# Kernel optimization log

Hardware: AMD Instinct MI355X
Metric: run time of the kernel (lower is better)

Reference implementation:

```python
import jax, jax.numpy as jnp
import numpy as np
import math

DT_SCALE = 1.0
DT_MIN, DT_MAX = 0.001, 0.1


def setup_inputs() -> dict:
    key = jax.random.key(0)
    ku, kdt, ka, kb, kc = jax.random.split(key, 5)
    batch, seq_len, d_model, d_state = 32, 4096, 256, 64
    u = jax.random.normal(ku, (batch, seq_len, d_model), dtype=jnp.float32)
    # log_dt ~ U[log(dt_min), log(dt_max)]
    log_dt = jax.random.uniform(kdt, (d_model,), dtype=jnp.float32) * (
        math.log(DT_MAX) - math.log(DT_MIN)) + math.log(DT_MIN)
    # A_real = -exp(U(-1, 1))  (strictly negative -> stable recurrence)
    A_real = -jnp.exp(jax.random.uniform(ka, (d_model, d_state), dtype=jnp.float32) * 2.0 - 1.0)
    B = jax.random.normal(kb, (d_model, d_state), dtype=jnp.float32)
    C = jax.random.normal(kc, (d_model, d_state), dtype=jnp.float32)
    x0 = jnp.zeros((d_model, d_state), dtype=jnp.float32)
    return {"u": u, "log_dt": log_dt, "A_real": A_real, "B": B, "C": C, "x0": x0}


def reference(u, log_dt, A_real, B, C, x0):
    # u: (batch, seq_len, d_model)
    batch = u.shape[0]
    dt = jnp.exp(log_dt) * DT_SCALE                      # (D,)
    A_tilde = jnp.exp(A_real * dt[:, None])              # (D, N)
    B_tilde = (1.0 - A_tilde) * B / A_real               # (D, N)
    x_init = jnp.broadcast_to(x0, (batch,) + x0.shape)   # (B, D, N)

    def step(x, u_t):
        # x: (B, D, N), u_t: (B, D)
        x = A_tilde * x + B_tilde * u_t[..., None]
        y = jnp.sum(C * x, axis=-1)                      # (B, D)
        return x, y

    u_t_major = jnp.swapaxes(u, 0, 1)                    # (L, B, D)
    _, ys = jax.lax.scan(step, x_init, u_t_major)        # ys: (L, B, D)
    return jnp.swapaxes(ys, 0, 1)                        # (B, L, D)
```

## Files before the change

### kernel.cpp

```cpp
#include <hip/hip_runtime.h>
#include <math.h>

#define BATCH 32
#define SEQ   4096
#define DM    256
#define NS    64
#define TSTEP 16


__global__ __launch_bounds__(256, 2)
void pass1_kernel(const float* __restrict__ u,
                  const float* __restrict__ log_dt,
                  const float* __restrict__ A_real,
                  float* __restrict__ S, int Tc) {
    __shared__ float tiles[4][2][TSTEP][16];
    int wid  = threadIdx.x >> 6;
    int lane = threadIdx.x & 63;
    int wave = (blockIdx.x * blockDim.x + threadIdx.x) >> 6;
    int w  = wave & 511;
    int g  = wave >> 9;
    int b  = w >> 4;
    int d0 = (w & 15) << 4;
    int c   = lane >> 2;
    int sub = lane & 3;
    int d   = d0 + c;
    int n0  = sub << 4;

    float a[16], z[16];
    {
        float dt = expf(log_dt[d]);
        const float* Ap = A_real + d * NS + n0;
#pragma unroll
        for (int k = 0; k < 16; ++k) {
            a[k] = expf(Ap[k] * dt);
            z[k] = 0.0f;
        }
    }

    const float* gsrc = u + (size_t)b * SEQ * DM + (size_t)(g * Tc) * DM
                        + (size_t)(lane >> 2) * DM + d0 + ((lane & 3) << 2);
    const size_t tadv = (size_t)TSTEP * DM;
    float* slot0 = &tiles[wid][0][0][0] + (lane << 2);
    const int ntiles = Tc / TSTEP;

    float4 rnext = *(const float4*)gsrc;
    *(float4*)slot0 = rnext;
    gsrc += tadv;
    rnext = *(const float4*)gsrc;
    gsrc += tadv;

    for (int tile = 0; tile < ntiles; ++tile) {
        int cur = tile & 1;
        if (tile + 1 < ntiles)
            *(float4*)(slot0 + (((tile + 1) & 1) << 8)) = rnext;
        if (tile + 2 < ntiles) {
            rnext = *(const float4*)gsrc;
            gsrc += tadv;
        }
        const float* tb = &tiles[wid][cur][0][0] + c;
#pragma unroll
        for (int s = 0; s < TSTEP; ++s) {
            float uv = tb[s << 4];
#pragma unroll
            for (int k = 0; k < 16; ++k)
                z[k] = fmaf(a[k], z[k], uv);
        }
    }

    float* Sp = S + (((size_t)g * BATCH + b) * DM + d) * NS + n0;
    float4* Sp4 = (float4*)Sp;
#pragma unroll
    for (int j = 0; j < 4; ++j)
        Sp4[j] = make_float4(z[4 * j], z[4 * j + 1], z[4 * j + 2], z[4 * j + 3]);
}

__global__ void pass2_kernel(float* __restrict__ S,
                             const float* __restrict__ log_dt,
                             const float* __restrict__ A_real,
                             const float* __restrict__ B,
                             const float* __restrict__ x0,
                             int C, int Tc) {
    int idx = blockIdx.x * blockDim.x + threadIdx.x;
    if (idx >= BATCH * DM * NS) return;
    int dn = idx & (DM * NS - 1);
    int d = dn >> 6;
    float ar = A_real[dn];
    float dt = expf(log_dt[d]);
    float aT = expf(ar * dt * (float)Tc);
    float x0v = x0[dn];
    float prev;
    if (x0v == 0.0f) {
        prev = 0.0f;
    } else {
        float at = expf(ar * dt);
        float bt = (1.0f - at) * B[dn] / ar;
        prev = (bt != 0.0f) ? (x0v / bt) : 0.0f;
    }
    const size_t stride = (size_t)BATCH * DM * NS;
    if (C == 16) {
        float v[15];
#pragma unroll
        for (int g = 0; g < 15; ++g) v[g] = S[(size_t)g * stride + idx];
#pragma unroll
        for (int g = 0; g < 15; ++g) {
            S[(size_t)g * stride + idx] = prev;
            prev = fmaf(aT, prev, v[g]);
        }
        S[15 * stride + idx] = prev;
    } else {
        for (int g = 0; g < C - 1; ++g) {
            float* p = S + (size_t)g * stride + idx;
            float s = *p;
            *p = prev;
            prev = fmaf(aT, prev, s);
        }
        S[(size_t)(C - 1) * stride + idx] = prev;
    }
}

__global__ __launch_bounds__(256, 2)
void pass3_kernel(const float* __restrict__ u,
                  const float* __restrict__ log_dt,
                  const float* __restrict__ A_real,
                  const float* __restrict__ B,
                  const float* __restrict__ Cm,
                  const float* __restrict__ S,
                  const float* __restrict__ x0,
                  float* __restrict__ y, int Tc, int useS) {
    __shared__ float tiles[4][2][TSTEP][16];
    int wid  = threadIdx.x >> 6;
    int lane = threadIdx.x & 63;
    int wave = (blockIdx.x * blockDim.x + threadIdx.x) >> 6;
    int w  = wave & 511;
    int g  = wave >> 9;
    int b  = w >> 4;
    int d0 = (w & 15) << 4;
    int c   = lane >> 2;
    int sub = lane & 3;
    int d   = d0 + c;
    int n0  = sub << 4;

    float a[16], cbt[16], z[16];
    {
        float dt = expf(log_dt[d]);
        const float* Ap = A_real + d * NS + n0;
        const float* Bp = B + d * NS + n0;
        const float* Cp = Cm + d * NS + n0;
#pragma unroll
        for (int k = 0; k < 16; ++k) {
            float ar = Ap[k];
            float at = expf(ar * dt);
            a[k] = at;
            cbt[k] = Cp[k] * ((1.0f - at) * Bp[k] / ar);
        }
        if (useS) {
            const float4* Sp4 = (const float4*)(S +
                (((size_t)g * BATCH + b) * DM + d) * NS + n0);
#pragma unroll
            for (int j = 0; j < 4; ++j) {
                float4 v = Sp4[j];
                z[4 * j] = v.x; z[4 * j + 1] = v.y;
                z[4 * j + 2] = v.z; z[4 * j + 3] = v.w;
            }
        } else {
            const float* Xp = x0 + d * NS + n0;
#pragma unroll
            for (int k = 0; k < 16; ++k) {
                float x0v = Xp[k];
                if (x0v == 0.0f) { z[k] = 0.0f; }
                else {
                    float bt = (1.0f - a[k]) * Bp[k] / Ap[k];
                    z[k] = (bt != 0.0f) ? (x0v / bt) : 0.0f;
                }
            }
        }
    }

    const float* gsrc = u + (size_t)b * SEQ * DM + (size_t)(g * Tc) * DM
                        + (size_t)(lane >> 2) * DM + d0 + ((lane & 3) << 2);
    const size_t tadv = (size_t)TSTEP * DM;
    float* slot0 = &tiles[wid][0][0][0] + (lane << 2);
    const int ntiles = Tc / TSTEP;
    float* yptr = y + (size_t)b * SEQ * DM + (size_t)(g * Tc) * DM + d;

    float4 rnext = *(const float4*)gsrc;
    *(float4*)slot0 = rnext;
    gsrc += tadv;
    rnext = *(const float4*)gsrc;
    gsrc += tadv;

    for (int tile = 0; tile < ntiles; ++tile) {
        int cur = tile & 1;
        if (tile + 1 < ntiles)
            *(float4*)(slot0 + (((tile + 1) & 1) << 8)) = rnext;
        if (tile + 2 < ntiles) {
            rnext = *(const float4*)gsrc;
            gsrc += tadv;
        }
        const float* tb = &tiles[wid][cur][0][0] + c;
#pragma unroll
        for (int s = 0; s < TSTEP; ++s) {
            float uv = tb[s << 4];
            float p0 = 0.0f, p1 = 0.0f;
#pragma unroll
            for (int k = 0; k < 16; k += 2) {
                z[k]     = fmaf(a[k],     z[k],     uv); p0 = fmaf(cbt[k],     z[k],     p0);
                z[k + 1] = fmaf(a[k + 1], z[k + 1], uv); p1 = fmaf(cbt[k + 1], z[k + 1], p1);
            }
            float p = p0 + p1;
            p += __shfl_xor(p, 1);
            p += __shfl_xor(p, 2);
            if (sub == 0) *yptr = p;
            yptr += DM;
        }
    }
}

extern "C" void kernel_launch(void* const* d_in, const int* in_sizes, int n_in,
                              void* d_out, int out_size, void* d_ws, size_t ws_size,
                              hipStream_t stream) {
    const float* u      = (const float*)d_in[0];
    const float* log_dt = (const float*)d_in[1];
    const float* A_real = (const float*)d_in[2];
    const float* B      = (const float*)d_in[3];
    const float* Cm     = (const float*)d_in[4];
    const float* x0     = (const float*)d_in[5];
    float* y = (float*)d_out;
    float* S = (float*)d_ws;

    const size_t per_chunk = (size_t)BATCH * DM * NS * sizeof(float);
    int C = 16;
    while (C > 1 && (size_t)C * per_chunk > ws_size) C >>= 1;
    if ((size_t)C * per_chunk > ws_size) C = 1;
    int Tc = SEQ / C;

    if (C > 1) {
        pass1_kernel<<<dim3((C - 1) * 128), dim3(256), 0, stream>>>(
            u, log_dt, A_real, S, Tc);
        pass2_kernel<<<dim3((BATCH * DM * NS) / 256), dim3(256), 0, stream>>>(
            S, log_dt, A_real, B, x0, C, Tc);
    }
    pass3_kernel<<<dim3(C * 128), dim3(256), 0, stream>>>(
        u, log_dt, A_real, B, Cm, S, x0, y, Tc, (C > 1) ? 1 : 0);
}
```

Before: 388.4 us.

## Fuse scan passes into one cooperative kernel with grid-wide sync

Adds a cooperative kernel that runs the chunk-summary pass, a grid sync, then a per-wave carry combine and the output pass. It drops the separate carry-propagation kernel and two extra launches. The price is redundant carry accumulation over earlier chunks in every wave and a grid barrier. It falls back to the three-kernel path when the occupancy check says all blocks cannot be co-resident.

Measured after the change: 397.7 us. 2.4% more time.

```diff
diff --git a/kernel.cpp b/kernel.cpp
--- a/kernel.cpp
+++ b/kernel.cpp
@@ -1,5 +1,8 @@
 #include <hip/hip_runtime.h>
+#include <hip/hip_cooperative_groups.h>
 #include <math.h>
+
+namespace cg = cooperative_groups;
 
 #define BATCH 32
 #define SEQ   4096
@@ -7,6 +10,155 @@
 #define NS    64
 #define TSTEP 16
 
+
+__global__ __launch_bounds__(256, 2)
+void fused_kernel(const float* __restrict__ u,
+                  const float* __restrict__ log_dt,
+                  const float* __restrict__ A_real,
+                  const float* __restrict__ B,
+                  const float* __restrict__ Cm,
+                  float* __restrict__ S,
+                  const float* __restrict__ x0,
+                  float* __restrict__ y, int Tc, int C) {
+    __shared__ float tiles[4][2][TSTEP][16];
+    int wid  = threadIdx.x >> 6;
+    int lane = threadIdx.x & 63;
+    int wave = (blockIdx.x * blockDim.x + threadIdx.x) >> 6;
+    int w  = wave & 511;
+    int g  = wave >> 9;
+    int b  = w >> 4;
+    int d0 = (w & 15) << 4;
+    int c   = lane >> 2;
+    int sub = lane & 3;
+    int d   = d0 + c;
+    int n0  = sub << 4;
+
+    float dt = expf(log_dt[d]);
+    const float* Ap = A_real + d * NS + n0;
+    float a[16], z[16];
+#pragma unroll
+    for (int k = 0; k < 16; ++k)
+        a[k] = expf(Ap[k] * dt);
+
+    const size_t tadv = (size_t)TSTEP * DM;
+    float* slot0 = &tiles[wid][0][0][0] + (lane << 2);
+    const int ntiles = Tc / TSTEP;
+    const size_t estride = (size_t)BATCH * DM * NS;
+
+    if (C > 1 && g < C - 1) {
+#pragma unroll
+        for (int k = 0; k < 16; ++k) z[k] = 0.0f;
+        const float* gsrc = u + (size_t)b * SEQ * DM + (size_t)(g * Tc) * DM
+                            + (size_t)(lane >> 2) * DM + d0 + ((lane & 3) << 2);
+        float4 rnext = *(const float4*)gsrc;
+        *(float4*)slot0 = rnext;
+        gsrc += tadv;
+        rnext = *(const float4*)gsrc;
+        gsrc += tadv;
+        for (int tile = 0; tile < ntiles; ++tile) {
+            int cur = tile & 1;
+            if (tile + 1 < ntiles)
+                *(float4*)(slot0 + (((tile + 1) & 1) << 8)) = rnext;
+            if (tile + 2 < ntiles) {
+                rnext = *(const float4*)gsrc;
+                gsrc += tadv;
+            }
+            const float* tb = &tiles[wid][cur][0][0] + c;
+#pragma unroll
+            for (int s = 0; s < TSTEP; ++s) {
+                float uv = tb[s << 4];
+#pragma unroll
+                for (int k = 0; k < 16; ++k)
+                    z[k] = fmaf(a[k], z[k], uv);
+            }
+        }
+        float* Sp = S + (((size_t)g * BATCH + b) * DM + d) * NS + n0;
+        float4* Sp4 = (float4*)Sp;
+#pragma unroll
+        for (int j = 0; j < 4; ++j)
+            Sp4[j] = make_float4(z[4*j], z[4*j+1], z[4*j+2], z[4*j+3]);
+    }
+
+    cg::this_grid().sync();
+
+    {
+        const float* Xp = x0 + d * NS + n0;
+        const float* Bp = B + d * NS + n0;
+#pragma unroll
+        for (int k = 0; k < 16; ++k) {
+            float x0v = Xp[k];
+            if (x0v == 0.0f) { z[k] = 0.0f; }
+            else {
+                float bt = (1.0f - a[k]) * Bp[k] / Ap[k];
+                z[k] = (bt != 0.0f) ? (x0v / bt) : 0.0f;
+            }
+        }
+    }
+    if (g > 0) {
+        float aT[16];
+        float dTc = dt * (float)Tc;
+#pragma unroll
+        for (int k = 0; k < 16; ++k)
+            aT[k] = expf(Ap[k] * dTc);
+        const float* Eb = S + ((size_t)b * DM + d) * NS + n0;
+        for (int h = 0; h < g; ++h) {
+            const float4* E4 = (const float4*)(Eb + (size_t)h * estride);
+            float e[16];
+#pragma unroll
+            for (int j = 0; j < 4; ++j) {
+                float4 v = E4[j];
+                e[4*j] = v.x; e[4*j+1] = v.y; e[4*j+2] = v.z; e[4*j+3] = v.w;
+            }
+#pragma unroll
+            for (int k = 0; k < 16; ++k)
+                z[k] = fmaf(aT[k], z[k], e[k]);
+        }
+    }
+
+    float cbt[16];
+    {
+        const float* Bp = B + d * NS + n0;
+        const float* Cp = Cm + d * NS + n0;
+#pragma unroll
+        for (int k = 0; k < 16; ++k)
+            cbt[k] = Cp[k] * ((1.0f - a[k]) * Bp[k] / Ap[k]);
+    }
+    const float* gsrc = u + (size_t)b * SEQ * DM + (size_t)(g * Tc) * DM
+                        + (size_t)(lane >> 2) * DM + d0 + ((lane & 3) << 2);
+    float* yptr = y + (size_t)b * SEQ * DM + (size_t)(g * Tc) * DM + d;
+
+    float4 rnext = *(const float4*)gsrc;
+    *(float4*)slot0 = rnext;
+    gsrc += tadv;
+    rnext = *(const float4*)gsrc;
+    gsrc += tadv;
+
+    for (int tile = 0; tile < ntiles; ++tile) {
+        int cur = tile & 1;
+        if (tile + 1 < ntiles)
+            *(float4*)(slot0 + (((tile + 1) & 1) << 8)) = rnext;
+        if (tile + 2 < ntiles) {
+            rnext = *(const float4*)gsrc;
+            gsrc += tadv;
+        }
+        const float* tb = &tiles[wid][cur][0][0] + c;
+#pragma unroll
+        for (int s = 0; s < TSTEP; ++s) {
+            float uv = tb[s << 4];
+            float p0 = 0.0f, p1 = 0.0f;
+#pragma unroll
+            for (int k = 0; k < 16; k += 2) {
+                z[k]   = fmaf(a[k],   z[k],   uv); p0 = fmaf(cbt[k],   z[k],   p0);
+                z[k+1] = fmaf(a[k+1], z[k+1], uv); p1 = fmaf(cbt[k+1], z[k+1], p1);
+            }
+            float p = p0 + p1;
+            p += __shfl_xor(p, 1);
+            p += __shfl_xor(p, 2);
+            if (sub == 0) yptr[s * DM] = p;
+        }
+        yptr += tadv;
+    }
+}
 
 __global__ __launch_bounds__(256, 2)
 void pass1_kernel(const float* __restrict__ u,
@@ -36,7 +188,6 @@
             z[k] = 0.0f;
         }
     }
-
     const float* gsrc = u + (size_t)b * SEQ * DM + (size_t)(g * Tc) * DM
                         + (size_t)(lane >> 2) * DM + d0 + ((lane & 3) << 2);
     const size_t tadv = (size_t)TSTEP * DM;
@@ -66,12 +217,11 @@
                 z[k] = fmaf(a[k], z[k], uv);
         }
     }
-
     float* Sp = S + (((size_t)g * BATCH + b) * DM + d) * NS + n0;
     float4* Sp4 = (float4*)Sp;
 #pragma unroll
     for (int j = 0; j < 4; ++j)
-        Sp4[j] = make_float4(z[4 * j], z[4 * j + 1], z[4 * j + 2], z[4 * j + 3]);
+        Sp4[j] = make_float4(z[4*j], z[4*j+1], z[4*j+2], z[4*j+3]);
 }
 
 __global__ void pass2_kernel(float* __restrict__ S,
@@ -159,8 +309,7 @@
 #pragma unroll
             for (int j = 0; j < 4; ++j) {
                 float4 v = Sp4[j];
-                z[4 * j] = v.x; z[4 * j + 1] = v.y;
-                z[4 * j + 2] = v.z; z[4 * j + 3] = v.w;
+                z[4*j] = v.x; z[4*j+1] = v.y; z[4*j+2] = v.z; z[4*j+3] = v.w;
             }
         } else {
             const float* Xp = x0 + d * NS + n0;
@@ -204,8 +353,8 @@
             float p0 = 0.0f, p1 = 0.0f;
 #pragma unroll
             for (int k = 0; k < 16; k += 2) {
-                z[k]     = fmaf(a[k],     z[k],     uv); p0 = fmaf(cbt[k],     z[k],     p0);
-                z[k + 1] = fmaf(a[k + 1], z[k + 1], uv); p1 = fmaf(cbt[k + 1], z[k + 1], p1);
+                z[k]   = fmaf(a[k],   z[k],   uv); p0 = fmaf(cbt[k],   z[k],   p0);
+                z[k+1] = fmaf(a[k+1], z[k+1], uv); p1 = fmaf(cbt[k+1], z[k+1], p1);
             }
             float p = p0 + p1;
             p += __shfl_xor(p, 1);
@@ -234,6 +383,35 @@
     if ((size_t)C * per_chunk > ws_size) C = 1;
     int Tc = SEQ / C;
 
+    static int coop_state = -1;
+    if (coop_state == -1) {
+        int ok = 0;
+        int dev = 0, nb = 0;
+        hipDeviceProp_t prop;
+        if (hipGetDevice(&dev) == hipSuccess &&
+            hipGetDeviceProperties(&prop, dev) == hipSuccess &&
+            hipOccupancyMaxActiveBlocksPerMultiprocessor(
+                &nb, (const void*)fused_kernel, 256, 0) == hipSuccess) {
+            if (prop.cooperativeLaunch &&
+                (long)nb * prop.multiProcessorCount >= (long)C * 128)
+                ok = 1;
+        }
+        (void)hipGetLastError();
+        coop_state = ok;
+    }
+
+    if (coop_state == 1) {
+        int aTc = Tc, aC = C;
+        void* args[] = {(void*)&u, (void*)&log_dt, (void*)&A_real, (void*)&B,
+                        (void*)&Cm, (void*)&S, (void*)&x0, (void*)&y,
+                        (void*)&aTc, (void*)&aC};
+        hipError_t err = hipLaunchCooperativeKernel(
+            (const void*)fused_kernel, dim3(C * 128), dim3(256), args, 0, stream);
+        if (err == hipSuccess) return;
+        (void)hipGetLastError();
+        coop_state = 0;
+    }
+
     if (C > 1) {
         pass1_kernel<<<dim3((C - 1) * 128), dim3(256), 0, stream>>>(
             u, log_dt, A_real, S, Tc);
```

## Fuse three-pass chunked scan into one kernel with inter-block flag synchronization

Applied to the files above, without the earlier changes.

Replaces the separate pass1/pass2/pass3 launches with a single kernel. Blocks take a dynamic virtual block id from an atomic counter, compute their chunk-end state, publish it with a flag, then wait on the flags of earlier chunks. Each block combines the earlier chunk states itself and runs the output scan. This removes two kernel launches and the separate sequential pass2, but adds spin-waiting, a memset, and a per-block combine of up to 15 chunk states read from global memory.

New measurement: 1.272 ms. 3.28x slower.

```diff
diff --git a/kernel.cpp b/kernel.cpp
--- a/kernel.cpp
+++ b/kernel.cpp
@@ -9,14 +9,26 @@
 
 
 __global__ __launch_bounds__(256, 2)
-void pass1_kernel(const float* __restrict__ u,
+void fused_kernel(const float* __restrict__ u,
                   const float* __restrict__ log_dt,
                   const float* __restrict__ A_real,
-                  float* __restrict__ S, int Tc) {
+                  const float* __restrict__ B,
+                  const float* __restrict__ Cm,
+                  float* __restrict__ S,
+                  const float* __restrict__ x0,
+                  float* __restrict__ y,
+                  unsigned int* __restrict__ flags,
+                  int Tc, int C) {
     __shared__ float tiles[4][2][TSTEP][16];
+    __shared__ int vbid_s;
+    if (threadIdx.x == 0)
+        vbid_s = (int)atomicAdd(&flags[31], 1u);
+    __syncthreads();
+    int vbid = vbid_s;
+
     int wid  = threadIdx.x >> 6;
     int lane = threadIdx.x & 63;
-    int wave = (blockIdx.x * blockDim.x + threadIdx.x) >> 6;
+    int wave = (vbid << 2) | wid;
     int w  = wave & 511;
     int g  = wave >> 9;
     int b  = w >> 4;
@@ -26,22 +38,102 @@
     int d   = d0 + c;
     int n0  = sub << 4;
 
+    float dt = expf(log_dt[d]);
+    const float* Ap = A_real + d * NS + n0;
     float a[16], z[16];
-    {
-        float dt = expf(log_dt[d]);
-        const float* Ap = A_real + d * NS + n0;
-#pragma unroll
-        for (int k = 0; k < 16; ++k) {
-            a[k] = expf(Ap[k] * dt);
-            z[k] = 0.0f;
-        }
-    }
-
-    const float* gsrc = u + (size_t)b * SEQ * DM + (size_t)(g * Tc) * DM
-                        + (size_t)(lane >> 2) * DM + d0 + ((lane & 3) << 2);
+#pragma unroll
+    for (int k = 0; k < 16; ++k)
+        a[k] = expf(Ap[k] * dt);
+
     const size_t tadv = (size_t)TSTEP * DM;
     float* slot0 = &tiles[wid][0][0][0] + (lane << 2);
     const int ntiles = Tc / TSTEP;
+    const size_t estride = (size_t)BATCH * DM * NS;
+
+    if (g < C - 1) {
+#pragma unroll
+        for (int k = 0; k < 16; ++k) z[k] = 0.0f;
+        const float* gsrc = u + (size_t)b * SEQ * DM + (size_t)(g * Tc) * DM
+                            + (size_t)(lane >> 2) * DM + d0 + ((lane & 3) << 2);
+        float4 rnext = *(const float4*)gsrc;
+        *(float4*)slot0 = rnext;
+        gsrc += tadv;
+        rnext = *(const float4*)gsrc;
+        gsrc += tadv;
+        for (int tile = 0; tile < ntiles; ++tile) {
+            int cur = tile & 1;
+            if (tile + 1 < ntiles)
+                *(float4*)(slot0 + (((tile + 1) & 1) << 8)) = rnext;
+            if (tile + 2 < ntiles) {
+                rnext = *(const float4*)gsrc;
+                gsrc += tadv;
+            }
+            const float* tb = &tiles[wid][cur][0][0] + c;
+#pragma unroll
+            for (int s = 0; s < TSTEP; ++s) {
+                float uv = tb[s << 4];
+#pragma unroll
+                for (int k = 0; k < 16; ++k)
+                    z[k] = fmaf(a[k], z[k], uv);
+            }
+        }
+        float* Sp = S + (((size_t)g * BATCH + b) * DM + d) * NS + n0;
+        float4* Sp4 = (float4*)Sp;
+#pragma unroll
+        for (int j = 0; j < 4; ++j)
+            Sp4[j] = make_float4(z[4*j], z[4*j+1], z[4*j+2], z[4*j+3]);
+        __threadfence();
+        if (lane == 0)
+            atomicAdd(&flags[g], 1u);
+    }
+
+    {
+        const float* Xp = x0 + d * NS + n0;
+        const float* Bp = B + d * NS + n0;
+#pragma unroll
+        for (int k = 0; k < 16; ++k) {
+            float x0v = Xp[k];
+            if (x0v == 0.0f) { z[k] = 0.0f; }
+            else {
+                float bt = (1.0f - a[k]) * Bp[k] / Ap[k];
+                z[k] = (bt != 0.0f) ? (x0v / bt) : 0.0f;
+            }
+        }
+    }
+    if (g > 0) {
+        float aT[16];
+        float dTc = dt * (float)Tc;
+#pragma unroll
+        for (int k = 0; k < 16; ++k)
+            aT[k] = expf(Ap[k] * dTc);
+        const float* Eb = S + ((size_t)b * DM + d) * NS + n0;
+        for (int h = 0; h < g; ++h) {
+            while (__hip_atomic_load(&flags[h], __ATOMIC_ACQUIRE,
+                                     __HIP_MEMORY_SCOPE_AGENT) < 512u)
+                __builtin_amdgcn_s_sleep(2);
+            const float4* E4 = (const float4*)(Eb + (size_t)h * estride);
+#pragma unroll
+            for (int j = 0; j < 4; ++j) {
+                float4 v = E4[j];
+                z[4*j]   = fmaf(aT[4*j],   z[4*j],   v.x);
+                z[4*j+1] = fmaf(aT[4*j+1], z[4*j+1], v.y);
+                z[4*j+2] = fmaf(aT[4*j+2], z[4*j+2], v.z);
+                z[4*j+3] = fmaf(aT[4*j+3], z[4*j+3], v.w);
+            }
+        }
+    }
+
+    float cbt[16];
+    {
+        const float* Bp = B + d * NS + n0;
+        const float* Cp = Cm + d * NS + n0;
+#pragma unroll
+        for (int k = 0; k < 16; ++k)
+            cbt[k] = Cp[k] * ((1.0f - a[k]) * Bp[k] / Ap[k]);
+    }
+    const float* gsrc = u + (size_t)b * SEQ * DM + (size_t)(g * Tc) * DM
+                        + (size_t)(lane >> 2) * DM + d0 + ((lane & 3) << 2);
+    float* yptr = y + (size_t)b * SEQ * DM + (size_t)(g * Tc) * DM + d;
 
     float4 rnext = *(const float4*)gsrc;
     *(float4*)slot0 = rnext;
@@ -61,78 +153,34 @@
 #pragma unroll
         for (int s = 0; s < TSTEP; ++s) {
             float uv = tb[s << 4];
-#pragma unroll
-            for (int k = 0; k < 16; ++k)
-                z[k] = fmaf(a[k], z[k], uv);
-        }
-    }
-
-    float* Sp = S + (((size_t)g * BATCH + b) * DM + d) * NS + n0;
-    float4* Sp4 = (float4*)Sp;
-#pragma unroll
-    for (int j = 0; j < 4; ++j)
-        Sp4[j] = make_float4(z[4 * j], z[4 * j + 1], z[4 * j + 2], z[4 * j + 3]);
+            float p0 = 0.0f, p1 = 0.0f;
+#pragma unroll
+            for (int k = 0; k < 16; k += 2) {
+                z[k]   = fmaf(a[k],   z[k],   uv); p0 = fmaf(cbt[k],   z[k],   p0);
+                z[k+1] = fmaf(a[k+1], z[k+1], uv); p1 = fmaf(cbt[k+1], z[k+1], p1);
+            }
+            float p = p0 + p1;
+            p += __shfl_xor(p, 1);
+            p += __shfl_xor(p, 2);
+            if (sub == 0) yptr[s * DM] = p;
+        }
+        yptr += tadv;
+    }
 }
 
-__global__ void pass2_kernel(float* __restrict__ S,
-                             const float* __restrict__ log_dt,
-                             const float* __restrict__ A_real,
-                             const float* __restrict__ B,
-                             const float* __restrict__ x0,
-                             int C, int Tc) {
-    int idx = blockIdx.x * blockDim.x + threadIdx.x;
-    if (idx >= BATCH * DM * NS) return;
-    int dn = idx & (DM * NS - 1);
-    int d = dn >> 6;
-    float ar = A_real[dn];
-    float dt = expf(log_dt[d]);
-    float aT = expf(ar * dt * (float)Tc);
-    float x0v = x0[dn];
-    float prev;
-    if (x0v == 0.0f) {
-        prev = 0.0f;
-    } else {
-        float at = expf(ar * dt);
-        float bt = (1.0f - at) * B[dn] / ar;
-        prev = (bt != 0.0f) ? (x0v / bt) : 0.0f;
-    }
-    const size_t stride = (size_t)BATCH * DM * NS;
-    if (C == 16) {
-        float v[15];
-#pragma unroll
-        for (int g = 0; g < 15; ++g) v[g] = S[(size_t)g * stride + idx];
-#pragma unroll
-        for (int g = 0; g < 15; ++g) {
-            S[(size_t)g * stride + idx] = prev;
-            prev = fmaf(aT, prev, v[g]);
-        }
-        S[15 * stride + idx] = prev;
-    } else {
-        for (int g = 0; g < C - 1; ++g) {
-            float* p = S + (size_t)g * stride + idx;
-            float s = *p;
-            *p = prev;
-            prev = fmaf(aT, prev, s);
-        }
-        S[(size_t)(C - 1) * stride + idx] = prev;
-    }
-}
-
 __global__ __launch_bounds__(256, 2)
-void pass3_kernel(const float* __restrict__ u,
+void scan1_kernel(const float* __restrict__ u,
                   const float* __restrict__ log_dt,
                   const float* __restrict__ A_real,
                   const float* __restrict__ B,
                   const float* __restrict__ Cm,
-                  const float* __restrict__ S,
                   const float* __restrict__ x0,
-                  float* __restrict__ y, int Tc, int useS) {
+                  float* __restrict__ y, int Tc) {
     __shared__ float tiles[4][2][TSTEP][16];
     int wid  = threadIdx.x >> 6;
     int lane = threadIdx.x & 63;
     int wave = (blockIdx.x * blockDim.x + threadIdx.x) >> 6;
     int w  = wave & 511;
-    int g  = wave >> 9;
     int b  = w >> 4;
     int d0 = (w & 15) << 4;
     int c   = lane >> 2;
@@ -146,42 +194,24 @@
         const float* Ap = A_real + d * NS + n0;
         const float* Bp = B + d * NS + n0;
         const float* Cp = Cm + d * NS + n0;
+        const float* Xp = x0 + d * NS + n0;
 #pragma unroll
         for (int k = 0; k < 16; ++k) {
             float ar = Ap[k];
             float at = expf(ar * dt);
             a[k] = at;
-            cbt[k] = Cp[k] * ((1.0f - at) * Bp[k] / ar);
-        }
-        if (useS) {
-            const float4* Sp4 = (const float4*)(S +
-                (((size_t)g * BATCH + b) * DM + d) * NS + n0);
-#pragma unroll
-            for (int j = 0; j < 4; ++j) {
-                float4 v = Sp4[j];
-                z[4 * j] = v.x; z[4 * j + 1] = v.y;
-                z[4 * j + 2] = v.z; z[4 * j + 3] = v.w;
-            }
-        } else {
-            const float* Xp = x0 + d * NS + n0;
-#pragma unroll
-            for (int k = 0; k < 16; ++k) {
-                float x0v = Xp[k];
-                if (x0v == 0.0f) { z[k] = 0.0f; }
-                else {
-                    float bt = (1.0f - a[k]) * Bp[k] / Ap[k];
-                    z[k] = (bt != 0.0f) ? (x0v / bt) : 0.0f;
-                }
-            }
-        }
-    }
-
-    const float* gsrc = u + (size_t)b * SEQ * DM + (size_t)(g * Tc) * DM
+            float bt = (1.0f - at) * Bp[k] / ar;
+            cbt[k] = Cp[k] * bt;
+            float x0v = Xp[k];
+            z[k] = (x0v == 0.0f) ? 0.0f : ((bt != 0.0f) ? (x0v / bt) : 0.0f);
+        }
+    }
+    const float* gsrc = u + (size_t)b * SEQ * DM
                         + (size_t)(lane >> 2) * DM + d0 + ((lane & 3) << 2);
     const size_t tadv = (size_t)TSTEP * DM;
     float* slot0 = &tiles[wid][0][0][0] + (lane << 2);
     const int ntiles = Tc / TSTEP;
-    float* yptr = y + (size_t)b * SEQ * DM + (size_t)(g * Tc) * DM + d;
+    float* yptr = y + (size_t)b * SEQ * DM + d;
 
     float4 rnext = *(const float4*)gsrc;
     *(float4*)slot0 = rnext;
@@ -204,15 +234,15 @@
             float p0 = 0.0f, p1 = 0.0f;
 #pragma unroll
             for (int k = 0; k < 16; k += 2) {
-                z[k]     = fmaf(a[k],     z[k],     uv); p0 = fmaf(cbt[k],     z[k],     p0);
-                z[k + 1] = fmaf(a[k + 1], z[k + 1], uv); p1 = fmaf(cbt[k + 1], z[k + 1], p1);
+                z[k]   = fmaf(a[k],   z[k],   uv); p0 = fmaf(cbt[k],   z[k],   p0);
+                z[k+1] = fmaf(a[k+1], z[k+1], uv); p1 = fmaf(cbt[k+1], z[k+1], p1);
             }
             float p = p0 + p1;
             p += __shfl_xor(p, 1);
             p += __shfl_xor(p, 2);
-            if (sub == 0) *yptr = p;
-            yptr += DM;
-        }
+            if (sub == 0) yptr[s * DM] = p;
+        }
+        yptr += tadv;
     }
 }
 
@@ -230,16 +260,18 @@
 
     const size_t per_chunk = (size_t)BATCH * DM * NS * sizeof(float);
     int C = 16;
-    while (C > 1 && (size_t)C * per_chunk > ws_size) C >>= 1;
-    if ((size_t)C * per_chunk > ws_size) C = 1;
+    while (C > 1 && (size_t)C * per_chunk + 256 > ws_size) C >>= 1;
+    if ((size_t)C * per_chunk + 256 > ws_size) C = 1;
     int Tc = SEQ / C;
 
     if (C > 1) {
-        pass1_kernel<<<dim3((C - 1) * 128), dim3(256), 0, stream>>>(
-            u, log_dt, A_real, S, Tc);
-        pass2_kernel<<<dim3((BATCH * DM * NS) / 256), dim3(256), 0, stream>>>(
-            S, log_dt, A_real, B, x0, C, Tc);
-    }
-    pass3_kernel<<<dim3(C * 128), dim3(256), 0, stream>>>(
-        u, log_dt, A_real, B, Cm, S, x0, y, Tc, (C > 1) ? 1 : 0);
+        unsigned int* flags =
+            (unsigned int*)((char*)d_ws + (size_t)C * per_chunk);
+        hipMemsetAsync(flags, 0, 32 * sizeof(unsigned int), stream);
+        fused_kernel<<<dim3(C * 128), dim3(256), 0, stream>>>(
+            u, log_dt, A_real, B, Cm, S, x0, y, flags, Tc, C);
+    } else {
+        scan1_kernel<<<dim3(128), dim3(256), 0, stream>>>(
+            u, log_dt, A_real, B, Cm, x0, y, Tc);
+    }
 }
```

## Fold chunk-carry combine into output pass and deepen u prefetch

Applied to the files above, without the earlier changes.

Removes the separate pass2 kernel that sequentially combined chunk end-states. Each pass3 wave now rebuilds its own starting state by folding all earlier chunk summaries, scaled by a^Tc, directly from workspace. This saves one launch and the workspace read-modify-write, at the cost of redundant per-wave reads and extra expf work in later chunks. Pass1 also prefetches u one tile further ahead in registers, and the workspace sizing now accounts for needing only C-1 chunk slots.

New measurement: 401.7 us. 1.03x slower.

```diff
diff --git a/kernel.cpp b/kernel.cpp
--- a/kernel.cpp
+++ b/kernel.cpp
@@ -43,21 +43,22 @@
     float* slot0 = &tiles[wid][0][0][0] + (lane << 2);
     const int ntiles = Tc / TSTEP;
 
-    float4 rnext = *(const float4*)gsrc;
-    *(float4*)slot0 = rnext;
-    gsrc += tadv;
-    rnext = *(const float4*)gsrc;
-    gsrc += tadv;
+    float4 r0 = *(const float4*)gsrc;
+    *(float4*)slot0 = r0;
+    float4 rA = *(const float4*)(gsrc + tadv);
+    float4 rB = *(const float4*)(gsrc + 2 * tadv);
+    gsrc += 3 * tadv;
 
     for (int tile = 0; tile < ntiles; ++tile) {
-        int cur = tile & 1;
-        if (tile + 1 < ntiles)
-            *(float4*)(slot0 + (((tile + 1) & 1) << 8)) = rnext;
-        if (tile + 2 < ntiles) {
-            rnext = *(const float4*)gsrc;
-            gsrc += tadv;
-        }
-        const float* tb = &tiles[wid][cur][0][0] + c;
+        if (tile + 1 < ntiles) {
+            *(float4*)(slot0 + (((tile + 1) & 1) << 8)) = rA;
+            rA = rB;
+            if (tile + 3 < ntiles) {
+                rB = *(const float4*)gsrc;
+                gsrc += tadv;
+            }
+        }
+        const float* tb = &tiles[wid][tile & 1][0][0] + c;
 #pragma unroll
         for (int s = 0; s < TSTEP; ++s) {
             float uv = tb[s << 4];
@@ -72,50 +73,6 @@
 #pragma unroll
     for (int j = 0; j < 4; ++j)
         Sp4[j] = make_float4(z[4 * j], z[4 * j + 1], z[4 * j + 2], z[4 * j + 3]);
-}
-
-__global__ void pass2_kernel(float* __restrict__ S,
-                             const float* __restrict__ log_dt,
-                             const float* __restrict__ A_real,
-                             const float* __restrict__ B,
-                             const float* __restrict__ x0,
-                             int C, int Tc) {
-    int idx = blockIdx.x * blockDim.x + threadIdx.x;
-    if (idx >= BATCH * DM * NS) return;
-    int dn = idx & (DM * NS - 1);
-    int d = dn >> 6;
-    float ar = A_real[dn];
-    float dt = expf(log_dt[d]);
-    float aT = expf(ar * dt * (float)Tc);
-    float x0v = x0[dn];
-    float prev;
-    if (x0v == 0.0f) {
-        prev = 0.0f;
-    } else {
-        float at = expf(ar * dt);
-        float bt = (1.0f - at) * B[dn] / ar;
-        prev = (bt != 0.0f) ? (x0v / bt) : 0.0f;
-    }
-    const size_t stride = (size_t)BATCH * DM * NS;
-    if (C == 16) {
-        float v[15];
-#pragma unroll
-        for (int g = 0; g < 15; ++g) v[g] = S[(size_t)g * stride + idx];
-#pragma unroll
-        for (int g = 0; g < 15; ++g) {
-            S[(size_t)g * stride + idx] = prev;
-            prev = fmaf(aT, prev, v[g]);
-        }
-        S[15 * stride + idx] = prev;
-    } else {
-        for (int g = 0; g < C - 1; ++g) {
-            float* p = S + (size_t)g * stride + idx;
-            float s = *p;
-            *p = prev;
-            prev = fmaf(aT, prev, s);
-        }
-        S[(size_t)(C - 1) * stride + idx] = prev;
-    }
 }
 
 __global__ __launch_bounds__(256, 2)
@@ -126,7 +83,7 @@
                   const float* __restrict__ Cm,
                   const float* __restrict__ S,
                   const float* __restrict__ x0,
-                  float* __restrict__ y, int Tc, int useS) {
+                  float* __restrict__ y, int Tc, int C) {
     __shared__ float tiles[4][2][TSTEP][16];
     int wid  = threadIdx.x >> 6;
     int lane = threadIdx.x & 63;
@@ -140,40 +97,52 @@
     int d   = d0 + c;
     int n0  = sub << 4;
 
-    float a[16], cbt[16], z[16];
+    float dt = expf(log_dt[d]);
+    const float* Ap = A_real + d * NS + n0;
+    const float* Bp = B + d * NS + n0;
+    float a[16], z[16];
+#pragma unroll
+    for (int k = 0; k < 16; ++k)
+        a[k] = expf(Ap[k] * dt);
+
+#pragma unroll
+    for (int k = 0; k < 16; ++k) {
+        float x0v = x0[d * NS + n0 + k];
+        if (x0v == 0.0f) { z[k] = 0.0f; }
+        else {
+            float bt = (1.0f - a[k]) * Bp[k] / Ap[k];
+            z[k] = (bt != 0.0f) ? (x0v / bt) : 0.0f;
+        }
+    }
+
+    if (g > 0) {
+        float aT[16];
+        float dTc = dt * (float)Tc;
+#pragma unroll
+        for (int k = 0; k < 16; ++k)
+            aT[k] = expf(Ap[k] * dTc);
+        const size_t estride = (size_t)BATCH * DM * NS;
+        const float* Eb = S + ((size_t)b * DM + d) * NS + n0;
+        for (int h = 0; h < g; ++h) {
+            const float4* E4 = (const float4*)(Eb + (size_t)h * estride);
+            float4 e0 = E4[0], e1 = E4[1], e2 = E4[2], e3 = E4[3];
+            z[0]  = fmaf(aT[0],  z[0],  e0.x); z[1]  = fmaf(aT[1],  z[1],  e0.y);
+            z[2]  = fmaf(aT[2],  z[2],  e0.z); z[3]  = fmaf(aT[3],  z[3],  e0.w);
+            z[4]  = fmaf(aT[4],  z[4],  e1.x); z[5]  = fmaf(aT[5],  z[5],  e1.y);
+            z[6]  = fmaf(aT[6],  z[6],  e1.z); z[7]  = fmaf(aT[7],  z[7],  e1.w);
+            z[8]  = fmaf(aT[8],  z[8],  e2.x); z[9]  = fmaf(aT[9],  z[9],  e2.y);
+            z[10] = fmaf(aT[10], z[10], e2.z); z[11] = fmaf(aT[11], z[11], e2.w);
+            z[12] = fmaf(aT[12], z[12], e3.x); z[13] = fmaf(aT[13], z[13], e3.y);
+            z[14] = fmaf(aT[14], z[14], e3.z); z[15] = fmaf(aT[15], z[15], e3.w);
+        }
+    }
+
+    float cbt[16];
     {
-        float dt = expf(log_dt[d]);
-        const float* Ap = A_real + d * NS + n0;
-        const float* Bp = B + d * NS + n0;
         const float* Cp = Cm + d * NS + n0;
 #pragma unroll
-        for (int k = 0; k < 16; ++k) {
-            float ar = Ap[k];
-            float at = expf(ar * dt);
-            a[k] = at;
-            cbt[k] = Cp[k] * ((1.0f - at) * Bp[k] / ar);
-        }
-        if (useS) {
-            const float4* Sp4 = (const float4*)(S +
-                (((size_t)g * BATCH + b) * DM + d) * NS + n0);
-#pragma unroll
-            for (int j = 0; j < 4; ++j) {
-                float4 v = Sp4[j];
-                z[4 * j] = v.x; z[4 * j + 1] = v.y;
-                z[4 * j + 2] = v.z; z[4 * j + 3] = v.w;
-            }
-        } else {
-            const float* Xp = x0 + d * NS + n0;
-#pragma unroll
-            for (int k = 0; k < 16; ++k) {
-                float x0v = Xp[k];
-                if (x0v == 0.0f) { z[k] = 0.0f; }
-                else {
-                    float bt = (1.0f - a[k]) * Bp[k] / Ap[k];
-                    z[k] = (bt != 0.0f) ? (x0v / bt) : 0.0f;
-                }
-            }
-        }
+        for (int k = 0; k < 16; ++k)
+            cbt[k] = Cp[k] * ((1.0f - a[k]) * Bp[k] / Ap[k]);
     }
 
     const float* gsrc = u + (size_t)b * SEQ * DM + (size_t)(g * Tc) * DM
@@ -204,15 +173,15 @@
             float p0 = 0.0f, p1 = 0.0f;
 #pragma unroll
             for (int k = 0; k < 16; k += 2) {
-                z[k]     = fmaf(a[k],     z[k],     uv); p0 = fmaf(cbt[k],     z[k],     p0);
-                z[k + 1] = fmaf(a[k + 1], z[k + 1], uv); p1 = fmaf(cbt[k + 1], z[k + 1], p1);
+                z[k]   = fmaf(a[k],   z[k],   uv); p0 = fmaf(cbt[k],   z[k],   p0);
+                z[k+1] = fmaf(a[k+1], z[k+1], uv); p1 = fmaf(cbt[k+1], z[k+1], p1);
             }
             float p = p0 + p1;
             p += __shfl_xor(p, 1);
             p += __shfl_xor(p, 2);
-            if (sub == 0) *yptr = p;
-            yptr += DM;
-        }
+            if (sub == 0) yptr[s * DM] = p;
+        }
+        yptr += tadv;
     }
 }
 
@@ -230,16 +199,14 @@
 
     const size_t per_chunk = (size_t)BATCH * DM * NS * sizeof(float);
     int C = 16;
-    while (C > 1 && (size_t)C * per_chunk > ws_size) C >>= 1;
-    if ((size_t)C * per_chunk > ws_size) C = 1;
+    while (C > 1 && (size_t)(C - 1) * per_chunk > ws_size) C >>= 1;
+    if ((size_t)(C - 1) * per_chunk > ws_size) C = 1;
     int Tc = SEQ / C;
 
     if (C > 1) {
         pass1_kernel<<<dim3((C - 1) * 128), dim3(256), 0, stream>>>(
             u, log_dt, A_real, S, Tc);
-        pass2_kernel<<<dim3((BATCH * DM * NS) / 256), dim3(256), 0, stream>>>(
-            S, log_dt, A_real, B, x0, C, Tc);
     }
     pass3_kernel<<<dim3(C * 128), dim3(256), 0, stream>>>(
-        u, log_dt, A_real, B, Cm, S, x0, y, Tc, (C > 1) ? 1 : 0);
+        u, log_dt, A_real, B, Cm, S, x0, y, Tc, C);
 }
```
